# Kernel tuning notes

Measured on AMD Instinct MI355X. Metric: run time of the kernel, lower is better.

## Reference

```python
import jax, jax.numpy as jnp
import numpy as np

B, N_IN, N_OUT, DEG = 128, 16384, 8192, 64
N_EDGES = N_OUT * DEG


def setup_inputs() -> dict:
    key = jax.random.key(0)
    k_x, k_src, k_dst, k_w = jax.random.split(key, 4)
    x = jax.random.normal(k_x, (B, N_IN), dtype=jnp.float32)
    # Ragged connectivity flattened to a CSR-like edge list:
    # edge_src[e] -> input feature index, edge_dst[e] -> output unit index.
    edge_src = jax.random.randint(k_src, (N_EDGES,), 0, N_IN, dtype=jnp.int64)
    edge_dst = jnp.sort(jax.random.randint(k_dst, (N_EDGES,), 0, N_OUT, dtype=jnp.int64))
    w = jax.random.normal(k_w, (N_EDGES,), dtype=jnp.float32) * 0.05  # one weight per edge
    bias = jnp.zeros((N_OUT,), dtype=jnp.float32)
    return {"x": x, "w": w, "bias": bias, "edge_src": edge_src, "edge_dst": edge_dst}


def reference(x, w, bias, edge_src, edge_dst):
    # Equivalent to: for each output j, y[:, j] = relu(x[:, edges_j] @ w_j + bias[j])
    # Vectorized as a single gather + weighted scatter-add over the flat edge list.
    n_out = bias.shape[0]
    gathered = x[:, edge_src] * w  # [B, E]
    y = jnp.zeros((x.shape[0], n_out), dtype=x.dtype).at[:, edge_dst].add(gathered)
    return jax.nn.relu(y + bias)
```

## Files before the change

kernel.cpp:

```cpp
#include <hip/hip_runtime.h>

#define B_DIM   128
#define N_IN    16384
#define N_OUT   8192
#define N_EDGES (N_OUT * 64)

#define WAVES_PB 8
#define J_BLK    WAVES_PB
#define THREADS  (WAVES_PB * 64)
#define CHUNK    64

__device__ __forceinline__ int lower_bound_dev(const int* __restrict__ a, int n, int v) {
    int lo = 0, hi = n;
    while (lo < hi) {
        int mid = (lo + hi) >> 1;
        if (a[mid] < v) lo = mid + 1; else hi = mid;
    }
    return lo;
}

__global__ void build_rowptr_kernel(const int* __restrict__ dst, int* __restrict__ rp) {
    const int e = blockIdx.x * blockDim.x + threadIdx.x;
    if (e >= N_EDGES) return;
    const int d     = dst[e];
    const int dprev = (e == 0) ? -1 : dst[e - 1];
    for (int j = dprev + 1; j <= d; ++j) rp[j] = e;
    if (e == N_EDGES - 1)
        for (int j = d + 1; j <= N_OUT; ++j) rp[j] = N_EDGES;
}

__global__ __launch_bounds__(256) void transpose_kernel(const float* __restrict__ x,
                                                        float* __restrict__ xT) {
    __shared__ float tile[32][33];
    const int i0 = blockIdx.x * 32;
    const int b0 = blockIdx.y * 32;
    const int tx = threadIdx.x;
    const int ty = threadIdx.y;
#pragma unroll
    for (int r = 0; r < 32; r += 8)
        tile[ty + r][tx] = x[(size_t)(b0 + ty + r) * N_IN + (i0 + tx)];
    __syncthreads();
#pragma unroll
    for (int r = 0; r < 32; r += 8)
        xT[(size_t)(i0 + ty + r) * B_DIM + (b0 + tx)] = tile[tx][ty + r];
}

template <bool TRANSPOSED, bool USE_RP>
__global__ __launch_bounds__(THREADS) void sparse_layer_kernel(
        const float* __restrict__ xg, const float* __restrict__ w,
        const float* __restrict__ bias, const int* __restrict__ src,
        const int* __restrict__ dst, const int* __restrict__ rp,
        float* __restrict__ y) {
    __shared__ int   s_src[J_BLK][CHUNK];
    __shared__ float s_w[J_BLK][CHUNK];
    __shared__ float tile[J_BLK][132];
    __shared__ int   srp[J_BLK + 1];

    const int tid  = threadIdx.x;
    const int wid  = tid >> 6;
    const int lane = tid & 63;
    const int j0   = blockIdx.x * J_BLK;
    const int j    = j0 + wid;

    if (!USE_RP) {
        if (tid <= J_BLK) srp[tid] = lower_bound_dev(dst, N_EDGES, j0 + tid);
        __syncthreads();
    }

    int e0, e1;
    if (USE_RP) { e0 = rp[j]; e1 = rp[j + 1]; }
    else        { e0 = srp[wid]; e1 = srp[wid + 1]; }

    float acc0 = 0.f, acc1 = 0.f;
    const int b0 = lane * 2;
    const float2* xrow = (const float2*)xg + lane;

    for (int base = e0; base < e1; base += CHUNK) {
        const int n = min(CHUNK, e1 - base);
        if (lane < n) {
            s_src[wid][lane] = src[base + lane];
            s_w[wid][lane]   = w[base + lane];
        }
        __builtin_amdgcn_wave_barrier();
#pragma unroll 4
        for (int k = 0; k < n; ++k) {
            const int   s  = s_src[wid][k];
            const float wt = s_w[wid][k];
            if (TRANSPOSED) {
                const float2 v = xrow[(size_t)s * (B_DIM / 2)];
                acc0 = fmaf(v.x, wt, acc0);
                acc1 = fmaf(v.y, wt, acc1);
            } else {
                acc0 = fmaf(xg[(size_t)b0 * N_IN + s],       wt, acc0);
                acc1 = fmaf(xg[(size_t)(b0 + 1) * N_IN + s], wt, acc1);
            }
        }
        __builtin_amdgcn_wave_barrier();
    }

    tile[wid][b0]     = acc0;
    tile[wid][b0 + 1] = acc1;
    __syncthreads();

#pragma unroll
    for (int i = tid; i < B_DIM * J_BLK; i += THREADS) {
        const int bb = i >> 3;
        const int jj = i & (J_BLK - 1);
        const float v = tile[jj][bb] + bias[j0 + jj];
        y[(size_t)bb * N_OUT + (j0 + jj)] = fmaxf(v, 0.f);
    }
}

extern "C" void kernel_launch(void* const* d_in, const int* in_sizes, int n_in,
                              void* d_out, int out_size, void* d_ws, size_t ws_size,
                              hipStream_t stream) {
    const float* x    = (const float*)d_in[0];
    const float* w    = (const float*)d_in[1];
    const float* bias = (const float*)d_in[2];
    const int*   esrc = (const int*)d_in[3];
    const int*   edst = (const int*)d_in[4];
    float*       y    = (float*)d_out;

    const size_t RP_BYTES = (size_t)(N_OUT + 1) * sizeof(int);
    const size_t XT_OFF   = 65536;
    const size_t XT_BYTES = (size_t)N_IN * B_DIM * sizeof(float);

    const bool has_rp = ws_size >= RP_BYTES;
    const bool has_xt = ws_size >= XT_OFF + XT_BYTES;

    int*   rp = (int*)d_ws;
    float* xT = (float*)((char*)d_ws + XT_OFF);

    if (has_rp) {
        build_rowptr_kernel<<<(N_EDGES + 255) / 256, 256, 0, stream>>>(edst, rp);
    }
    if (has_xt) {
        transpose_kernel<<<dim3(N_IN / 32, B_DIM / 32), dim3(32, 8), 0, stream>>>(x, xT);
    }

    dim3 grid(N_OUT / J_BLK);
    if (has_xt) {
        sparse_layer_kernel<true,  true ><<<grid, THREADS, 0, stream>>>(xT, w, bias, esrc, edst, rp, y);
    } else if (has_rp) {
        sparse_layer_kernel<false, true ><<<grid, THREADS, 0, stream>>>(x,  w, bias, esrc, edst, rp, y);
    } else {
        sparse_layer_kernel<false, false><<<grid, THREADS, 0, stream>>>(x,  w, bias, esrc, edst, rp, y);
    }
}
```

Before: 99.23 us.

## Split each wave into two half-waves loading float4 rows of transposed x

The fast path now has each half of a wave handle a different edge. Each lane loads a float4 (four batch columns) from the transposed x row, and the two halves are combined at the end with a cross-half shuffle. Edge indices and weights are read straight from global memory (uniform loads) instead of being staged through LDS with wave barriers, and the edge range is made wave-uniform with readfirstlane. The intent is more memory-level parallelism per wave and fewer LDS and instruction overheads. The cost is an extra shuffle reduction and an odd-edge tail loop.

```diff
diff --git a/kernel.cpp b/kernel.cpp
--- a/kernel.cpp
+++ b/kernel.cpp
@@ -8,7 +8,6 @@
 #define WAVES_PB 8
 #define J_BLK    WAVES_PB
 #define THREADS  (WAVES_PB * 64)
-#define CHUNK    64
 
 __device__ __forceinline__ int lower_bound_dev(const int* __restrict__ a, int n, int v) {
     int lo = 0, hi = n;
@@ -45,63 +44,105 @@
         xT[(size_t)(i0 + ty + r) * B_DIM + (b0 + tx)] = tile[tx][ty + r];
 }
 
-template <bool TRANSPOSED, bool USE_RP>
-__global__ __launch_bounds__(THREADS) void sparse_layer_kernel(
-        const float* __restrict__ xg, const float* __restrict__ w,
+__global__ __launch_bounds__(THREADS, 8) void sparse_layer_fast(
+        const float* __restrict__ xT, const float* __restrict__ w,
         const float* __restrict__ bias, const int* __restrict__ src,
-        const int* __restrict__ dst, const int* __restrict__ rp,
-        float* __restrict__ y) {
-    __shared__ int   s_src[J_BLK][CHUNK];
-    __shared__ float s_w[J_BLK][CHUNK];
+        const int* __restrict__ rp, float* __restrict__ y) {
     __shared__ float tile[J_BLK][132];
+
+    const int tid  = threadIdx.x;
+    const int wid  = tid >> 6;
+    const int lane = tid & 63;
+    const int half = lane >> 5;
+    const int bcol = (lane & 31) << 2;
+    const int j0   = blockIdx.x * J_BLK;
+    const int j    = j0 + wid;
+
+    const int e0 = __builtin_amdgcn_readfirstlane(rp[j]);
+    const int e1 = __builtin_amdgcn_readfirstlane(rp[j + 1]);
+
+    float4 acc = {0.f, 0.f, 0.f, 0.f};
+    const float4* xrow = (const float4*)xT + (bcol >> 2);
+
+    int e = e0;
+    for (; e + 8 <= e1; e += 8) {
+#pragma unroll
+        for (int p = 0; p < 4; ++p) {
+            const int   ea = e + 2 * p;
+            const int   sa = src[ea];
+            const int   sb = src[ea + 1];
+            const float wa = w[ea];
+            const float wb = w[ea + 1];
+            const int   s  = half ? sb : sa;
+            const float wt = half ? wb : wa;
+            const float4 v = xrow[(size_t)s * (B_DIM / 4)];
+            acc.x = fmaf(v.x, wt, acc.x);
+            acc.y = fmaf(v.y, wt, acc.y);
+            acc.z = fmaf(v.z, wt, acc.z);
+            acc.w = fmaf(v.w, wt, acc.w);
+        }
+    }
+    for (; e < e1; e += 2) {
+        const int   sa    = src[e];
+        const float wa    = w[e];
+        const bool  has_b = (e + 1) < e1;
+        const int   sb    = has_b ? src[e + 1] : sa;
+        const float wb    = has_b ? w[e + 1] : 0.f;
+        const int   s     = half ? sb : sa;
+        const float wt    = half ? wb : wa;
+        const float4 v = xrow[(size_t)s * (B_DIM / 4)];
+        acc.x = fmaf(v.x, wt, acc.x);
+        acc.y = fmaf(v.y, wt, acc.y);
+        acc.z = fmaf(v.z, wt, acc.z);
+        acc.w = fmaf(v.w, wt, acc.w);
+    }
+
+    acc.x += __shfl_xor(acc.x, 32, 64);
+    acc.y += __shfl_xor(acc.y, 32, 64);
+    acc.z += __shfl_xor(acc.z, 32, 64);
+    acc.w += __shfl_xor(acc.w, 32, 64);
+
+    if (half == 0) {
+        *(float4*)&tile[wid][bcol] = acc;
+    }
+    __syncthreads();
+
+#pragma unroll
+    for (int i = tid; i < B_DIM * J_BLK; i += THREADS) {
+        const int bb = i >> 3;
+        const int jj = i & (J_BLK - 1);
+        const float v = tile[jj][bb] + bias[j0 + jj];
+        y[(size_t)bb * N_OUT + (j0 + jj)] = fmaxf(v, 0.f);
+    }
+}
+
+__global__ __launch_bounds__(THREADS) void sparse_layer_fallback(
+        const float* __restrict__ x, const float* __restrict__ w,
+        const float* __restrict__ bias, const int* __restrict__ src,
+        const int* __restrict__ dst, float* __restrict__ y) {
+    __shared__ float tile[J_BLK][130];
     __shared__ int   srp[J_BLK + 1];
 
     const int tid  = threadIdx.x;
     const int wid  = tid >> 6;
     const int lane = tid & 63;
     const int j0   = blockIdx.x * J_BLK;
-    const int j    = j0 + wid;
 
-    if (!USE_RP) {
-        if (tid <= J_BLK) srp[tid] = lower_bound_dev(dst, N_EDGES, j0 + tid);
-        __syncthreads();
+    if (tid <= J_BLK) srp[tid] = lower_bound_dev(dst, N_EDGES, j0 + tid);
+    __syncthreads();
+
+    const int e0 = srp[wid], e1 = srp[wid + 1];
+    const int b0 = lane * 2;
+    float acc0 = 0.f, acc1 = 0.f;
+    for (int e = e0; e < e1; ++e) {
+        const int   s  = src[e];
+        const float wt = w[e];
+        acc0 = fmaf(x[(size_t)b0 * N_IN + s], wt, acc0);
+        acc1 = fmaf(x[(size_t)(b0 + 1) * N_IN + s], wt, acc1);
     }
-
-    int e0, e1;
-    if (USE_RP) { e0 = rp[j]; e1 = rp[j + 1]; }
-    else        { e0 = srp[wid]; e1 = srp[wid + 1]; }
-
-    float acc0 = 0.f, acc1 = 0.f;
-    const int b0 = lane * 2;
-    const float2* xrow = (const float2*)xg + lane;
-
-    for (int base = e0; base < e1; base += CHUNK) {
-        const int n = min(CHUNK, e1 - base);
-        if (lane < n) {
-            s_src[wid][lane] = src[base + lane];
-            s_w[wid][lane]   = w[base + lane];
-        }
-        __builtin_amdgcn_wave_barrier();
-#pragma unroll 4
-        for (int k = 0; k < n; ++k) {
-            const int   s  = s_src[wid][k];
-            const float wt = s_w[wid][k];
-            if (TRANSPOSED) {
-                const float2 v = xrow[(size_t)s * (B_DIM / 2)];
-                acc0 = fmaf(v.x, wt, acc0);
-                acc1 = fmaf(v.y, wt, acc1);
-            } else {
-                acc0 = fmaf(xg[(size_t)b0 * N_IN + s],       wt, acc0);
-                acc1 = fmaf(xg[(size_t)(b0 + 1) * N_IN + s], wt, acc1);
-            }
-        }
-        __builtin_amdgcn_wave_barrier();
-    }
-
     tile[wid][b0]     = acc0;
     tile[wid][b0 + 1] = acc1;
     __syncthreads();
-
 #pragma unroll
     for (int i = tid; i < B_DIM * J_BLK; i += THREADS) {
         const int bb = i >> 3;
@@ -125,25 +166,16 @@
     const size_t XT_OFF   = 65536;
     const size_t XT_BYTES = (size_t)N_IN * B_DIM * sizeof(float);
 
-    const bool has_rp = ws_size >= RP_BYTES;
-    const bool has_xt = ws_size >= XT_OFF + XT_BYTES;
+    const bool has_ws = ws_size >= XT_OFF + XT_BYTES && ws_size >= RP_BYTES;
 
     int*   rp = (int*)d_ws;
     float* xT = (float*)((char*)d_ws + XT_OFF);
 
-    if (has_rp) {
+    if (has_ws) {
         build_rowptr_kernel<<<(N_EDGES + 255) / 256, 256, 0, stream>>>(edst, rp);
-    }
-    if (has_xt) {
         transpose_kernel<<<dim3(N_IN / 32, B_DIM / 32), dim3(32, 8), 0, stream>>>(x, xT);
-    }
-
-    dim3 grid(N_OUT / J_BLK);
-    if (has_xt) {
-        sparse_layer_kernel<true,  true ><<<grid, THREADS, 0, stream>>>(xT, w, bias, esrc, edst, rp, y);
-    } else if (has_rp) {
-        sparse_layer_kernel<false, true ><<<grid, THREADS, 0, stream>>>(x,  w, bias, esrc, edst, rp, y);
+        sparse_layer_fast<<<dim3(N_OUT / J_BLK), THREADS, 0, stream>>>(xT, w, bias, esrc, rp, y);
     } else {
-        sparse_layer_kernel<false, false><<<grid, THREADS, 0, stream>>>(x,  w, bias, esrc, edst, rp, y);
+        sparse_layer_fallback<<<dim3(N_OUT / J_BLK), THREADS, 0, stream>>>(x, w, bias, esrc, edst, y);
     }
 }
```

Measured after the change: 98.81 us. Within noise of the previous version (-0.4%).
